# Performance work log

Hardware: AMD Instinct MI355X
Metric: run time of the kernel (lower is better)

Reference implementation:

```python
import jax, jax.numpy as jnp
import numpy as np

N, C, H, W = 16, 64, 128, 128
KH, KW = 3, 3
SH, SW = 1, 1


def _window_flat_indices(H, W):
    """Flat input indices of each element of each sliding window.
    Returns int32 array [num_windows, KH*KW]."""
    Ho = (H - KH) // SH + 1
    Wo = (W - KW) // SW + 1
    i = np.arange(Ho) * SH
    j = np.arange(Wo) * SW
    a = np.arange(KH)
    b = np.arange(KW)
    rows = i[:, None, None, None] + a[None, None, :, None]   # [Ho,1,KH,1]
    cols = j[None, :, None, None] + b[None, None, None, :]   # [1,Wo,1,KW]
    flat = (rows * W + cols).reshape(Ho * Wo, KH * KW)       # [Wn, K]
    return jnp.asarray(flat, dtype=jnp.int32)


def setup_inputs() -> dict:
    key = jax.random.key(0)
    x = jax.random.normal(key, (N, C, H, W), dtype=jnp.float32)
    return {"x": x}


def reference(x):
    n, c, h, w = x.shape
    flat = _window_flat_indices(h, w)            # [Wn, K]
    Wn, K = flat.shape
    nc = n * c
    xf = x.reshape(nc, h * w)                    # [NC, HW]
    patches = xf[:, flat]                        # [NC, Wn, K]
    amax = jnp.argmax(patches, axis=-1)          # [NC, Wn] local winner
    amin = jnp.argmin(patches, axis=-1)          # [NC, Wn]
    warp = jnp.arange(Wn)[None, :]
    win_max = flat[warp, amax]                   # [NC, Wn] flat input idx of max winner
    win_min = flat[warp, amin]                   # [NC, Wn]
    idx = jnp.concatenate([win_max, win_min], axis=1)                      # [NC, 2Wn]
    vals = jnp.concatenate([jnp.ones((Wn,), x.dtype), -jnp.ones((Wn,), x.dtype)])
    counts = jnp.zeros((nc, h * w), x.dtype)
    counts = counts.at[jnp.arange(nc)[:, None], idx].add(vals[None, :])
    return counts.reshape(n, c, h, w)
```

## Files before the change

kernel.cpp:

```cpp
#include <hip/hip_runtime.h>


#define HH 128
#define WW 128
#define HO 126
#define WO 126
#define PLANE (HH * WW)
#define NPLANES (16 * 64)
#define BLOCK 1024

__global__ __launch_bounds__(BLOCK, 8)
void energy_pool2d_kernel(const float* __restrict__ x, float* __restrict__ out) {
    __shared__ int cnt[PLANE];

    const int tid = threadIdx.x;
    const int plane = blockIdx.x;
    const float* __restrict__ xp = x + (size_t)plane * PLANE;

    int4* c4 = (int4*)cnt;
#pragma unroll
    for (int i = 0; i < PLANE / 4 / BLOCK; ++i)
        c4[tid + i * BLOCK] = make_int4(0, 0, 0, 0);
    __syncthreads();

    const int rt = tid >> 5;
    const int ct = tid & 31;
    const int wr0 = rt * 4;
    const int j0 = ct * 4;
    const bool cfull = (ct < 31);
    const bool rfull = (rt < 31);
    const int base = wr0 * WW + j0;
    const float* __restrict__ p = xp + base;

    float r[6][8];
#pragma unroll
    for (int q = 0; q < 6; ++q) {
        const int qs = (q >= 4 && !rfull) ? 3 : q;
        const float* rowp = p + qs * WW;
        const float4 a = *(const float4*)(rowp);
        const float4 b = *(const float4*)(rowp + (cfull ? 4 : 0));
        r[q][0] = a.x; r[q][1] = a.y; r[q][2] = a.z; r[q][3] = a.w;
        r[q][4] = b.x; r[q][5] = b.y; r[q][6] = b.z; r[q][7] = b.w;
    }

#pragma unroll
    for (int o = 0; o < 4; ++o) {
        float hM[6], hm[6];
        int hA[6], ha[6];
#pragma unroll
        for (int q = 0; q < 6; ++q) {
            const float v0 = r[q][o], v1 = r[q][o + 1], v2 = r[q][o + 2];
            const int f0 = q * WW + o;
            float M = fmaxf(fmaxf(v0, v1), v2);
            int A = f0 + 2;
            if (v1 == M) A = f0 + 1;
            if (v0 == M) A = f0;
            float m = fminf(fminf(v0, v1), v2);
            int a = f0 + 2;
            if (v1 == m) a = f0 + 1;
            if (v0 == m) a = f0;
            hM[q] = M; hA[q] = A; hm[q] = m; ha[q] = a;
        }
        const bool oval = (o < 2) || cfull;
#pragma unroll
        for (int q = 0; q < 4; ++q) {
            const bool qval = (q < 2) || rfull;
            if (oval && qval) {
                const float WM = fmaxf(fmaxf(hM[q], hM[q + 1]), hM[q + 2]);
                int wA = hA[q + 2];
                if (hM[q + 1] == WM) wA = hA[q + 1];
                if (hM[q] == WM) wA = hA[q];
                const float Wm = fminf(fminf(hm[q], hm[q + 1]), hm[q + 2]);
                int wa = ha[q + 2];
                if (hm[q + 1] == Wm) wa = ha[q + 1];
                if (hm[q] == Wm) wa = ha[q];
                atomicAdd(&cnt[base + wA], 1);
                atomicAdd(&cnt[base + wa], -1);
            }
        }
    }
    __syncthreads();

    float4* __restrict__ o4 = (float4*)(out + (size_t)plane * PLANE);
#pragma unroll
    for (int i = 0; i < PLANE / 4 / BLOCK; ++i) {
        const int4 ci = c4[tid + i * BLOCK];
        o4[tid + i * BLOCK] =
            make_float4((float)ci.x, (float)ci.y, (float)ci.z, (float)ci.w);
    }
}

extern "C" void kernel_launch(void* const* d_in, const int* in_sizes, int n_in,
                              void* d_out, int out_size, void* d_ws, size_t ws_size,
                              hipStream_t stream) {
    const float* x = (const float*)d_in[0];
    float* out = (float*)d_out;
    energy_pool2d_kernel<<<NPLANES, BLOCK, 0, stream>>>(x, out);
}
```

Before: 38.33 us.

## Shrink per-thread tile to 2x4 windows with a strided loop over 63 row tiles

Each thread now handles a 2-row by 4-column window tile, loading 4 input rows instead of 6, and loops over 2016 tiles with a block-stride loop. The aim is lower register pressure and fewer wasted clamped loads at the bottom edge. In exchange, vertical reuse drops because each thread loads 4 rows to produce 2 output rows instead of 6 rows for 4. About half the threads also run a second loop iteration, which adds imbalance within each block.

```diff
diff --git a/kernel.cpp b/kernel.cpp
--- a/kernel.cpp
+++ b/kernel.cpp
@@ -8,6 +8,9 @@
 #define PLANE (HH * WW)
 #define NPLANES (16 * 64)
 #define BLOCK 1024
+#define CTILES 32
+#define RTILES 63
+#define NTILES (CTILES * RTILES)
 
 __global__ __launch_bounds__(BLOCK, 8)
 void energy_pool2d_kernel(const float* __restrict__ x, float* __restrict__ out) {
@@ -23,59 +26,80 @@
         c4[tid + i * BLOCK] = make_int4(0, 0, 0, 0);
     __syncthreads();
 
-    const int rt = tid >> 5;
-    const int ct = tid & 31;
-    const int wr0 = rt * 4;
-    const int j0 = ct * 4;
-    const bool cfull = (ct < 31);
-    const bool rfull = (rt < 31);
-    const int base = wr0 * WW + j0;
-    const float* __restrict__ p = xp + base;
+    for (int t = tid; t < NTILES; t += BLOCK) {
+        const int rt = t >> 5;
+        const int ct = t & 31;
+        const int wr0 = rt * 2;
+        const int j0 = ct * 4;
+        const float* __restrict__ p = xp + wr0 * WW + j0;
+        const bool cfull = (ct < CTILES - 1);
 
-    float r[6][8];
+        float r[4][8];
+        const float4 a0 = *(const float4*)(p);
+        const float4 a1 = *(const float4*)(p + WW);
+        const float4 a2 = *(const float4*)(p + 2 * WW);
+        const float4 a3 = *(const float4*)(p + 3 * WW);
+        r[0][0] = a0.x; r[0][1] = a0.y; r[0][2] = a0.z; r[0][3] = a0.w;
+        r[1][0] = a1.x; r[1][1] = a1.y; r[1][2] = a1.z; r[1][3] = a1.w;
+        r[2][0] = a2.x; r[2][1] = a2.y; r[2][2] = a2.z; r[2][3] = a2.w;
+        r[3][0] = a3.x; r[3][1] = a3.y; r[3][2] = a3.z; r[3][3] = a3.w;
+        if (cfull) {
+            const float4 b0 = *(const float4*)(p + 4);
+            const float4 b1 = *(const float4*)(p + WW + 4);
+            const float4 b2 = *(const float4*)(p + 2 * WW + 4);
+            const float4 b3 = *(const float4*)(p + 3 * WW + 4);
+            r[0][4] = b0.x; r[0][5] = b0.y; r[0][6] = b0.z; r[0][7] = b0.w;
+            r[1][4] = b1.x; r[1][5] = b1.y; r[1][6] = b1.z; r[1][7] = b1.w;
+            r[2][4] = b2.x; r[2][5] = b2.y; r[2][6] = b2.z; r[2][7] = b2.w;
+            r[3][4] = b3.x; r[3][5] = b3.y; r[3][6] = b3.z; r[3][7] = b3.w;
+        } else {
 #pragma unroll
-    for (int q = 0; q < 6; ++q) {
-        const int qs = (q >= 4 && !rfull) ? 3 : q;
-        const float* rowp = p + qs * WW;
-        const float4 a = *(const float4*)(rowp);
-        const float4 b = *(const float4*)(rowp + (cfull ? 4 : 0));
-        r[q][0] = a.x; r[q][1] = a.y; r[q][2] = a.z; r[q][3] = a.w;
-        r[q][4] = b.x; r[q][5] = b.y; r[q][6] = b.z; r[q][7] = b.w;
-    }
+            for (int q = 0; q < 4; ++q)
+                r[q][4] = r[q][5] = r[q][6] = r[q][7] = 0.f;
+        }
 
-#pragma unroll
-    for (int o = 0; o < 4; ++o) {
-        float hM[6], hm[6];
-        int hA[6], ha[6];
-#pragma unroll
-        for (int q = 0; q < 6; ++q) {
-            const float v0 = r[q][o], v1 = r[q][o + 1], v2 = r[q][o + 2];
-            const int f0 = q * WW + o;
-            float M = fmaxf(fmaxf(v0, v1), v2);
-            int A = f0 + 2;
-            if (v1 == M) A = f0 + 1;
-            if (v0 == M) A = f0;
-            float m = fminf(fminf(v0, v1), v2);
-            int a = f0 + 2;
-            if (v1 == m) a = f0 + 1;
-            if (v0 == m) a = f0;
-            hM[q] = M; hA[q] = A; hm[q] = m; ha[q] = a;
-        }
-        const bool oval = (o < 2) || cfull;
+        const int base = wr0 * WW + j0;
+
+        float hM[4][4], hm[4][4];
+        int hA[4][4], ha[4][4];
 #pragma unroll
         for (int q = 0; q < 4; ++q) {
-            const bool qval = (q < 2) || rfull;
-            if (oval && qval) {
-                const float WM = fmaxf(fmaxf(hM[q], hM[q + 1]), hM[q + 2]);
-                int wA = hA[q + 2];
-                if (hM[q + 1] == WM) wA = hA[q + 1];
-                if (hM[q] == WM) wA = hA[q];
-                const float Wm = fminf(fminf(hm[q], hm[q + 1]), hm[q + 2]);
-                int wa = ha[q + 2];
-                if (hm[q + 1] == Wm) wa = ha[q + 1];
-                if (hm[q] == Wm) wa = ha[q];
-                atomicAdd(&cnt[base + wA], 1);
-                atomicAdd(&cnt[base + wa], -1);
+#pragma unroll
+            for (int o = 0; o < 4; ++o) {
+                const float v0 = r[q][o], v1 = r[q][o + 1], v2 = r[q][o + 2];
+                const int f0 = q * WW + o;
+                const float M = fmaxf(fmaxf(v0, v1), v2);
+                int A = f0 + 2;
+                if (v1 == M) A = f0 + 1;
+                if (v0 == M) A = f0;
+                const float m = fminf(fminf(v0, v1), v2);
+                int a = f0 + 2;
+                if (v1 == m) a = f0 + 1;
+                if (v0 == m) a = f0;
+                hM[q][o] = M; hA[q][o] = A;
+                hm[q][o] = m; ha[q][o] = a;
+            }
+        }
+
+        const int nw = cfull ? 4 : 2;
+#pragma unroll
+        for (int o = 0; o < 4; ++o) {
+            if (o < nw) {
+#pragma unroll
+                for (int wr = 0; wr < 2; ++wr) {
+                    const float WM =
+                        fmaxf(fmaxf(hM[wr][o], hM[wr + 1][o]), hM[wr + 2][o]);
+                    int wA = hA[wr + 2][o];
+                    if (hM[wr + 1][o] == WM) wA = hA[wr + 1][o];
+                    if (hM[wr][o] == WM) wA = hA[wr][o];
+                    const float Wm =
+                        fminf(fminf(hm[wr][o], hm[wr + 1][o]), hm[wr + 2][o]);
+                    int wa = ha[wr + 2][o];
+                    if (hm[wr + 1][o] == Wm) wa = ha[wr + 1][o];
+                    if (hm[wr][o] == Wm) wa = ha[wr][o];
+                    atomicAdd(&cnt[base + wA], 1);
+                    atomicAdd(&cnt[base + wa], -1);
+                }
             }
         }
     }
```

Measured after the change: 81.94 us. 114% more time.

## Split each plane across two blocks with half-size LDS histograms

Applied to the files above, without the earlier changes.

Each plane is processed by two 512-thread blocks, each covering half the rows and owning a 64-row LDS counter buffer. Winners outside a block's half are discarded, so windows near the seam are computed redundantly by both blocks. This halves per-block shared memory and doubles the grid, aiming to raise occupancy and overlap of load/compute/store phases at the cost of some duplicated work and extra bounds checks.

```diff
diff --git a/kernel.cpp b/kernel.cpp
--- a/kernel.cpp
+++ b/kernel.cpp
@@ -6,84 +6,100 @@
 #define HO 126
 #define WO 126
 #define PLANE (HH * WW)
+#define HROWS 64
+#define HPLANE (HROWS * WW)
 #define NPLANES (16 * 64)
-#define BLOCK 1024
+#define BLOCK 512
 
-__global__ __launch_bounds__(BLOCK, 8)
+__global__ __launch_bounds__(BLOCK, 4)
 void energy_pool2d_kernel(const float* __restrict__ x, float* __restrict__ out) {
-    __shared__ int cnt[PLANE];
+    __shared__ int cnt[HPLANE];
 
     const int tid = threadIdx.x;
-    const int plane = blockIdx.x;
+    const int plane = blockIdx.x >> 1;
+    const int half = blockIdx.x & 1;
     const float* __restrict__ xp = x + (size_t)plane * PLANE;
 
     int4* c4 = (int4*)cnt;
 #pragma unroll
-    for (int i = 0; i < PLANE / 4 / BLOCK; ++i)
+    for (int i = 0; i < HPLANE / 4 / BLOCK; ++i)
         c4[tid + i * BLOCK] = make_int4(0, 0, 0, 0);
     __syncthreads();
 
+    const int row0 = half ? 62 : 0;
+    const int bias = half * HPLANE;
+
     const int rt = tid >> 5;
     const int ct = tid & 31;
-    const int wr0 = rt * 4;
+    const int wr0 = row0 + rt * 4;
     const int j0 = ct * 4;
+    const float* __restrict__ p = xp + wr0 * WW + j0;
     const bool cfull = (ct < 31);
-    const bool rfull = (rt < 31);
-    const int base = wr0 * WW + j0;
-    const float* __restrict__ p = xp + base;
 
     float r[6][8];
 #pragma unroll
     for (int q = 0; q < 6; ++q) {
-        const int qs = (q >= 4 && !rfull) ? 3 : q;
-        const float* rowp = p + qs * WW;
-        const float4 a = *(const float4*)(rowp);
-        const float4 b = *(const float4*)(rowp + (cfull ? 4 : 0));
+        const float4 a = *(const float4*)(p + q * WW);
         r[q][0] = a.x; r[q][1] = a.y; r[q][2] = a.z; r[q][3] = a.w;
-        r[q][4] = b.x; r[q][5] = b.y; r[q][6] = b.z; r[q][7] = b.w;
     }
+    if (cfull) {
+#pragma unroll
+        for (int q = 0; q < 6; ++q) {
+            const float4 b = *(const float4*)(p + q * WW + 4);
+            r[q][4] = b.x; r[q][5] = b.y; r[q][6] = b.z; r[q][7] = b.w;
+        }
+    } else {
+#pragma unroll
+        for (int q = 0; q < 6; ++q)
+            r[q][4] = r[q][5] = r[q][6] = r[q][7] = 0.f;
+    }
+
+    const int base = wr0 * WW + j0;
 
 #pragma unroll
     for (int o = 0; o < 4; ++o) {
+        const bool oval = (o < 2) || cfull;
         float hM[6], hm[6];
         int hA[6], ha[6];
 #pragma unroll
         for (int q = 0; q < 6; ++q) {
             const float v0 = r[q][o], v1 = r[q][o + 1], v2 = r[q][o + 2];
             const int f0 = q * WW + o;
-            float M = fmaxf(fmaxf(v0, v1), v2);
+            const float M = fmaxf(fmaxf(v0, v1), v2);
             int A = f0 + 2;
             if (v1 == M) A = f0 + 1;
             if (v0 == M) A = f0;
-            float m = fminf(fminf(v0, v1), v2);
+            const float m = fminf(fminf(v0, v1), v2);
             int a = f0 + 2;
             if (v1 == m) a = f0 + 1;
             if (v0 == m) a = f0;
             hM[q] = M; hA[q] = A; hm[q] = m; ha[q] = a;
         }
-        const bool oval = (o < 2) || cfull;
 #pragma unroll
-        for (int q = 0; q < 4; ++q) {
-            const bool qval = (q < 2) || rfull;
-            if (oval && qval) {
-                const float WM = fmaxf(fmaxf(hM[q], hM[q + 1]), hM[q + 2]);
-                int wA = hA[q + 2];
-                if (hM[q + 1] == WM) wA = hA[q + 1];
-                if (hM[q] == WM) wA = hA[q];
-                const float Wm = fminf(fminf(hm[q], hm[q + 1]), hm[q + 2]);
-                int wa = ha[q + 2];
-                if (hm[q + 1] == Wm) wa = ha[q + 1];
-                if (hm[q] == Wm) wa = ha[q];
-                atomicAdd(&cnt[base + wA], 1);
-                atomicAdd(&cnt[base + wa], -1);
+        for (int wr = 0; wr < 4; ++wr) {
+            if (oval) {
+                const float WM =
+                    fmaxf(fmaxf(hM[wr], hM[wr + 1]), hM[wr + 2]);
+                int wA = hA[wr + 2];
+                if (hM[wr + 1] == WM) wA = hA[wr + 1];
+                if (hM[wr] == WM) wA = hA[wr];
+                const float Wm =
+                    fminf(fminf(hm[wr], hm[wr + 1]), hm[wr + 2]);
+                int wa = ha[wr + 2];
+                if (hm[wr + 1] == Wm) wa = ha[wr + 1];
+                if (hm[wr] == Wm) wa = ha[wr];
+                const int iM = base + wA - bias;
+                if ((unsigned)iM < HPLANE) atomicAdd(&cnt[iM], 1);
+                const int im = base + wa - bias;
+                if ((unsigned)im < HPLANE) atomicAdd(&cnt[im], -1);
             }
         }
     }
     __syncthreads();
 
-    float4* __restrict__ o4 = (float4*)(out + (size_t)plane * PLANE);
+    float4* __restrict__ o4 = (float4*)(out + (size_t)plane * PLANE + bias);
 #pragma unroll
-    for (int i = 0; i < PLANE / 4 / BLOCK; ++i) {
+    for (int i = 0; i < HPLANE / 4 / BLOCK; ++i) {
         const int4 ci = c4[tid + i * BLOCK];
         o4[tid + i * BLOCK] =
             make_float4((float)ci.x, (float)ci.y, (float)ci.z, (float)ci.w);
@@ -95,5 +111,5 @@
                               hipStream_t stream) {
     const float* x = (const float*)d_in[0];
     float* out = (float*)d_out;
-    energy_pool2d_kernel<<<NPLANES, BLOCK, 0, stream>>>(x, out);
+    energy_pool2d_kernel<<<NPLANES * 2, BLOCK, 0, stream>>>(x, out);
 }
```

New measurement: 33.13 us. 13.5% less time.
